# Kernel tuning notes

Measured on AMD Instinct MI355X. Metric: run time of the kernel, lower is better.

## Reference

```python
import jax, jax.numpy as jnp
import numpy as np
from fractions import Fraction
from math import factorial

MUL = 128
LS = [0, 1, 2]  # Rs_in1 = Rs_in2 = [(128,0),(128,1),(128,2)]
D_IN = MUL * sum(2 * l + 1 for l in LS)  # 1152
D_OUT = MUL * sum(2 * lo + 1 for l in LS for lo in range(2 * l + 1))  # 4480
N = 16384


def _su2_cg(j1, m1, j2, m2, j3, m3):
    # SU(2) Clebsch-Gordan coefficient (Racah formula), exact rational arithmetic.
    if m3 != m1 + m2:
        return 0.0
    f = lambda n: factorial(round(n))
    vmin = int(max(-j1 + j2 + m3, -j1 + m1, 0))
    vmax = int(min(j2 + j3 + m1, j3 - j1 + j2, j3 + m3))
    c = ((2.0 * j3 + 1.0) * Fraction(
        f(j3 + j1 - j2) * f(j3 - j1 + j2) * f(j1 + j2 - j3) * f(j3 + m3) * f(j3 - m3),
        f(j1 + j2 + j3 + 1) * f(j1 - m1) * f(j1 + m1) * f(j2 - m2) * f(j2 + m2))) ** 0.5
    s = 0
    for v in range(vmin, vmax + 1):
        s += (-1) ** (v + j2 + m2) * Fraction(
            f(j2 + j3 + m1 - v) * f(j1 - m1 + v),
            f(v) * f(j3 - j1 + j2 - v) * f(j3 + m3 - v) * f(v + j1 - j2 - m3))
    return float(c * s)


def _su2_tensor(j1, j2, j3):
    C = np.zeros((2 * j1 + 1, 2 * j2 + 1, 2 * j3 + 1))
    for m1 in range(-j1, j1 + 1):
        for m2 in range(-j2, j2 + 1):
            m3 = m1 + m2
            if abs(m3) <= j3:
                C[j1 + m1, j2 + m2, j3 + m3] = _su2_cg(j1, m1, j2, m2, j3, m3)
    return C


def _cb(l):
    # change of basis real -> complex spherical harmonics (e3nn convention, incl. (-i)^l phase)
    q = np.zeros((2 * l + 1, 2 * l + 1), dtype=np.complex128)
    for m in range(-l, 0):
        q[l + m, l + abs(m)] = 2 ** -0.5
        q[l + m, l - abs(m)] = -1j * 2 ** -0.5
    q[l, l] = 1.0
    for m in range(1, l + 1):
        q[l + m, l + abs(m)] = (-1) ** m * 2 ** -0.5
        q[l + m, l - abs(m)] = 1j * (-1) ** m * 2 ** -0.5
    return (-1j) ** l * q


def _wigner3j(l1, l2, l3):
    # real-basis Wigner 3j tensor, unit Frobenius norm (e3nn convention)
    C = _su2_tensor(l1, l2, l3).astype(np.complex128)
    C = np.einsum('ij,kl,mn,ikn->jlm', _cb(l1), _cb(l2), np.conj(_cb(l3).T), C)
    C = np.real(C)
    return C / np.linalg.norm(C)


# precomputed CG blocks with 'component' normalization: w3j(l_out, l, l) * sqrt(2*l_out+1)
CG = {(lo, l): jnp.asarray((_wigner3j(lo, l, l) * np.sqrt(2 * lo + 1)).astype(np.float32))
      for l in LS for lo in range(2 * l + 1)}


def _forward(features_1, features_2):
    # elementwise (channel-matched) tensor product, block-sparse CG contraction.
    # Equivalent to: outer(features_1, features_2) then sparse Wigner-3j mixing matmul,
    # but without materializing the [N, d1, d2] outer product.
    lead = features_1.shape[:-1]
    outs = []
    off = 0
    for l in LS:
        d = MUL * (2 * l + 1)
        b1 = features_1[..., off:off + d].reshape(*lead, MUL, 2 * l + 1)
        b2 = features_2[..., off:off + d].reshape(*lead, MUL, 2 * l + 1)
        for lo in range(2 * l + 1):  # selection_rule: l_out in |l-l|..2l, ascending
            o = jnp.einsum('kij,...ui,...uj->...uk', CG[(lo, l)], b1, b2)
            outs.append(o.reshape(*lead, MUL * (2 * lo + 1)))
        off += d
    return jnp.concatenate(outs, axis=-1)  # [..., D_OUT]


def setup_inputs() -> dict:
    key = jax.random.key(0)
    k1, k2 = jax.random.split(key)
    return {
        "features_1": jax.random.normal(k1, (N, D_IN), dtype=jnp.float32),
        "features_2": jax.random.normal(k2, (N, D_IN), dtype=jnp.float32),
    }


def reference(features_1, features_2):
    return _forward(features_1, features_2)
```

## Files before the change

kernel.cpp:

```cpp
#include <hip/hip_runtime.h>


#define NROW 16384
#define DIN  1152
#define DOUT 4480

__device__ float g_cgtab[707];

struct cd { double x, y; };
__device__ __forceinline__ cd cmul(cd a, cd b) {
    return cd{a.x * b.x - a.y * b.y, a.x * b.y + a.y * b.x};
}

__device__ __forceinline__ int imax(int a, int b) { return a > b ? a : b; }
__device__ __forceinline__ int imin(int a, int b) { return a < b ? a : b; }

__device__ double su2_cg_d(int j1, int m1, int j2, int m2, int j3, int m3,
                           const double* f) {
    if (m3 != m1 + m2) return 0.0;
    int vmin = imax(imax(-j1 + j2 + m3, -j1 + m1), 0);
    int vmax = imin(imin(j2 + j3 + m1, j3 - j1 + j2), j3 + m3);
    if (vmax < vmin) return 0.0;
    double c = sqrt((2.0 * j3 + 1.0) *
                    f[j3 + j1 - j2] * f[j3 - j1 + j2] * f[j1 + j2 - j3] *
                    f[j3 + m3] * f[j3 - m3] /
                    (f[j1 + j2 + j3 + 1] * f[j1 - m1] * f[j1 + m1] *
                     f[j2 - m2] * f[j2 + m2]));
    double s = 0.0;
    for (int v = vmin; v <= vmax; ++v) {
        double num = f[j2 + j3 + m1 - v] * f[j1 - m1 + v];
        double den = f[v] * f[j3 - j1 + j2 - v] * f[j3 + m3 - v] * f[v + j1 - j2 - m3];
        double term = num / den;
        s += ((v + j2 + m2) & 1) ? -term : term;
    }
    return c * s;
}

__device__ void fill_cb(int l, cd* q) {
    int d = 2 * l + 1;
    for (int i = 0; i < d * d; i++) q[i] = cd{0.0, 0.0};
    const double is2 = 0.70710678118654752440;
    for (int m = -l; m < 0; m++) {
        q[(l + m) * d + (l - m)] = cd{is2, 0.0};
        q[(l + m) * d + (l + m)] = cd{0.0, -is2};
    }
    q[l * d + l] = cd{1.0, 0.0};
    for (int m = 1; m <= l; m++) {
        double sg = (m & 1) ? -1.0 : 1.0;
        q[(l + m) * d + (l + m)] = cd{sg * is2, 0.0};
        q[(l + m) * d + (l - m)] = cd{0.0, sg * is2};
    }
    int ph = l & 3;
    for (int i = 0; i < d * d; i++) {
        cd z = q[i], r;
        if (ph == 0) r = z;
        else if (ph == 1) r = cd{z.y, -z.x};
        else if (ph == 2) r = cd{-z.x, -z.y};
        else r = cd{-z.y, z.x};
        q[i] = r;
    }
}

__global__ void cg_gen() {
    int b = blockIdx.x;
    int l = (b == 0) ? 0 : (b < 4 ? 1 : 2);
    int lo = (b == 0) ? 0 : (b < 4 ? b - 1 : b - 4);
    int base = (l == 0) ? 0 : (l == 1 ? 1 : 82);
    int d2 = 2 * l + 1, d1 = 2 * lo + 1;
    int off = base + d2 * d2 * lo * lo;
    int Nent = d1 * d2 * d2;

    __shared__ double fct[12];
    __shared__ double su2[225];
    __shared__ cd cb1[81];
    __shared__ cd cb2[25];
    __shared__ double val[225];

    if (threadIdx.x == 0) {
        fct[0] = 1.0;
        for (int i = 1; i < 12; i++) fct[i] = fct[i - 1] * i;
    }
    __syncthreads();

    for (int e = threadIdx.x; e < Nent; e += blockDim.x) {
        int i = e / (d2 * d2), r = e % (d2 * d2);
        int k = r / d2, n = r % d2;
        su2[e] = su2_cg_d(lo, i - lo, l, k - l, l, n - l, fct);
    }
    if (threadIdx.x == 0) { fill_cb(lo, cb1); fill_cb(l, cb2); }
    __syncthreads();

    for (int e = threadIdx.x; e < Nent; e += blockDim.x) {
        int jo = e / (d2 * d2), r = e % (d2 * d2);
        int kb = r / d2, mb = r % d2;
        double sx = 0.0;
        for (int i = 0; i < d1; i++) {
            cd c1 = cb1[i * d1 + jo];
            for (int k = 0; k < d2; k++) {
                cd c12 = cmul(c1, cb2[k * d2 + kb]);
                for (int n = 0; n < d2; n++) {
                    double cv = su2[(i * d2 + k) * d2 + n];
                    if (cv != 0.0) {
                        cd c3 = cb2[n * d2 + mb];
                        c3.y = -c3.y;
                        cd term = cmul(c12, c3);
                        sx += term.x * cv;
                    }
                }
            }
        }
        val[e] = sx;
    }
    __syncthreads();

    double ss = 0.0;
    for (int e = 0; e < Nent; e++) { double v = val[e]; ss += v * v; }
    double scale = sqrt((double)d1) / sqrt(ss);
    for (int e = threadIdx.x; e < Nent; e += blockDim.x)
        g_cgtab[off + e] = (float)(val[e] * scale);
}


template <int DO_, int NE>
__device__ __forceinline__ void contractP(const float* __restrict__ t,
                                          const float* q,
                                          float* __restrict__ os) {
#pragma unroll
    for (int k = 0; k < DO_; k++) {
        float acc = 0.0f;
#pragma unroll
        for (int e = 0; e < NE; e++) acc = fmaf(t[k * NE + e], q[e], acc);
        os[k] = acc;
    }
}

__global__ __launch_bounds__(256, 6) void etp_main(
    const float* __restrict__ f1, const float* __restrict__ f2,
    float* __restrict__ out) {
    __shared__ alignas(16) float os[4096];
    const float* __restrict__ t = g_cgtab;

    const int tid = threadIdx.x;
    const int ch = tid & 127;
    const size_t row = blockIdx.x;

    const float* __restrict__ p1 = f1 + row * DIN;
    const float* __restrict__ p2 = f2 + row * DIN;
    float* __restrict__ po = out + row * DOUT;

    if (tid < 128) {
        float a0 = p1[ch], b0 = p2[ch];
        float a1[3], b1[3];
#pragma unroll
        for (int k = 0; k < 3; k++) {
            a1[k] = p1[128 + ch * 3 + k];
            b1[k] = p2[128 + ch * 3 + k];
        }
        float a2[5], b2[5];
#pragma unroll
        for (int k = 0; k < 5; k++) {
            a2[k] = p1[512 + ch * 5 + k];
            b2[k] = p2[512 + ch * 5 + k];
        }

        po[ch] = t[0] * a0 * b0;

        float q1[9];
#pragma unroll
        for (int i = 0; i < 3; i++)
#pragma unroll
            for (int j = 0; j < 3; j++) q1[i * 3 + j] = a1[i] * b1[j];
        {
            float s = 0.0f;
#pragma unroll
            for (int e = 0; e < 9; e++) s = fmaf(t[1 + e], q1[e], s);
            po[128 + ch] = s;
        }
        contractP<3, 9>(t + 10, q1, os + 0 + ch * 3);
        contractP<5, 9>(t + 37, q1, os + 384 + ch * 5);

        float q2[25];
#pragma unroll
        for (int i = 0; i < 5; i++)
#pragma unroll
            for (int j = 0; j < 5; j++) q2[i * 5 + j] = a2[i] * b2[j];
        contractP<9, 25>(t + 482, q2, os + 2944 + ch * 9);
    } else {
        float a2[5], b2[5];
#pragma unroll
        for (int k = 0; k < 5; k++) {
            a2[k] = p1[512 + ch * 5 + k];
            b2[k] = p2[512 + ch * 5 + k];
        }
        float q2[25];
#pragma unroll
        for (int i = 0; i < 5; i++)
#pragma unroll
            for (int j = 0; j < 5; j++) q2[i * 5 + j] = a2[i] * b2[j];
        {
            float s = 0.0f;
#pragma unroll
            for (int e = 0; e < 25; e++) s = fmaf(t[82 + e], q2[e], s);
            po[1280 + ch] = s;
        }
        contractP<3, 25>(t + 107, q2, os + 1024 + ch * 3);
        contractP<5, 25>(t + 182, q2, os + 1408 + ch * 5);
        contractP<7, 25>(t + 307, q2, os + 2048 + ch * 7);
    }

    __syncthreads();

    const float4* __restrict__ src = reinterpret_cast<const float4*>(os);
    float4* __restrict__ dA = reinterpret_cast<float4*>(po + 256);
    float4* __restrict__ dB = reinterpret_cast<float4*>(po + 1408);
    dA[tid] = src[tid];
#pragma unroll
    for (int i = 1; i < 4; i++) dB[tid + 256 * (i - 1)] = src[tid + 256 * i];
}

extern "C" void kernel_launch(void* const* d_in, const int* in_sizes, int n_in,
                              void* d_out, int out_size, void* d_ws, size_t ws_size,
                              hipStream_t stream) {
    const float* f1 = (const float*)d_in[0];
    const float* f2 = (const float*)d_in[1];
    float* out = (float*)d_out;

    hipLaunchKernelGGL(cg_gen, dim3(9), dim3(256), 0, stream);
    hipLaunchKernelGGL(etp_main, dim3(NROW), dim3(256), 0, stream,
                       f1, f2, out);
}
```

Measured before the change: 428.2 us.

## Compute CG table on host and rebalance per-thread work in main kernel

Replaces the device-side cg_gen kernel with a host computation of the 707-entry CG table, copied asynchronously into the device symbol before the main launch. This removes a small serial GPU kernel from the timed stream, adding a small H2D copy and host work instead. In etp_main, the l=2 input loads and outer product now run in both halves of the block, and the l_out=0 contraction of the l=2 block moves from the upper 128 threads to the lower 128. This evens out the FMA count between the two thread halves.

```diff
diff --git a/kernel.cpp b/kernel.cpp
--- a/kernel.cpp
+++ b/kernel.cpp
@@ -1,4 +1,5 @@
 #include <hip/hip_runtime.h>
+#include <cmath>
 
 
 #define NROW 16384
@@ -7,25 +8,28 @@
 
 __device__ float g_cgtab[707];
 
+namespace cghost {
+
 struct cd { double x, y; };
-__device__ __forceinline__ cd cmul(cd a, cd b) {
+static inline cd cmul(cd a, cd b) {
     return cd{a.x * b.x - a.y * b.y, a.x * b.y + a.y * b.x};
 }
-
-__device__ __forceinline__ int imax(int a, int b) { return a > b ? a : b; }
-__device__ __forceinline__ int imin(int a, int b) { return a < b ? a : b; }
-
-__device__ double su2_cg_d(int j1, int m1, int j2, int m2, int j3, int m3,
-                           const double* f) {
+static inline int imax(int a, int b) { return a > b ? a : b; }
+static inline int imin(int a, int b) { return a < b ? a : b; }
+
+static double fct[12];
+
+static double su2_cg(int j1, int m1, int j2, int m2, int j3, int m3) {
     if (m3 != m1 + m2) return 0.0;
+    const double* f = fct;
     int vmin = imax(imax(-j1 + j2 + m3, -j1 + m1), 0);
     int vmax = imin(imin(j2 + j3 + m1, j3 - j1 + j2), j3 + m3);
     if (vmax < vmin) return 0.0;
-    double c = sqrt((2.0 * j3 + 1.0) *
-                    f[j3 + j1 - j2] * f[j3 - j1 + j2] * f[j1 + j2 - j3] *
-                    f[j3 + m3] * f[j3 - m3] /
-                    (f[j1 + j2 + j3 + 1] * f[j1 - m1] * f[j1 + m1] *
-                     f[j2 - m2] * f[j2 + m2]));
+    double c = std::sqrt((2.0 * j3 + 1.0) *
+                         f[j3 + j1 - j2] * f[j3 - j1 + j2] * f[j1 + j2 - j3] *
+                         f[j3 + m3] * f[j3 - m3] /
+                         (f[j1 + j2 + j3 + 1] * f[j1 - m1] * f[j1 + m1] *
+                          f[j2 - m2] * f[j2 + m2]));
     double s = 0.0;
     for (int v = vmin; v <= vmax; ++v) {
         double num = f[j2 + j3 + m1 - v] * f[j1 - m1 + v];
@@ -36,7 +40,7 @@
     return c * s;
 }
 
-__device__ void fill_cb(int l, cd* q) {
+static void fill_cb(int l, cd* q) {
     int d = 2 * l + 1;
     for (int i = 0; i < d * d; i++) q[i] = cd{0.0, 0.0};
     const double is2 = 0.70710678118654752440;
@@ -61,64 +65,62 @@
     }
 }
 
-__global__ void cg_gen() {
-    int b = blockIdx.x;
-    int l = (b == 0) ? 0 : (b < 4 ? 1 : 2);
-    int lo = (b == 0) ? 0 : (b < 4 ? b - 1 : b - 4);
-    int base = (l == 0) ? 0 : (l == 1 ? 1 : 82);
-    int d2 = 2 * l + 1, d1 = 2 * lo + 1;
-    int off = base + d2 * d2 * lo * lo;
-    int Nent = d1 * d2 * d2;
-
-    __shared__ double fct[12];
-    __shared__ double su2[225];
-    __shared__ cd cb1[81];
-    __shared__ cd cb2[25];
-    __shared__ double val[225];
-
-    if (threadIdx.x == 0) {
-        fct[0] = 1.0;
-        for (int i = 1; i < 12; i++) fct[i] = fct[i - 1] * i;
-    }
-    __syncthreads();
-
-    for (int e = threadIdx.x; e < Nent; e += blockDim.x) {
-        int i = e / (d2 * d2), r = e % (d2 * d2);
-        int k = r / d2, n = r % d2;
-        su2[e] = su2_cg_d(lo, i - lo, l, k - l, l, n - l, fct);
-    }
-    if (threadIdx.x == 0) { fill_cb(lo, cb1); fill_cb(l, cb2); }
-    __syncthreads();
-
-    for (int e = threadIdx.x; e < Nent; e += blockDim.x) {
-        int jo = e / (d2 * d2), r = e % (d2 * d2);
-        int kb = r / d2, mb = r % d2;
-        double sx = 0.0;
-        for (int i = 0; i < d1; i++) {
-            cd c1 = cb1[i * d1 + jo];
-            for (int k = 0; k < d2; k++) {
-                cd c12 = cmul(c1, cb2[k * d2 + kb]);
-                for (int n = 0; n < d2; n++) {
-                    double cv = su2[(i * d2 + k) * d2 + n];
-                    if (cv != 0.0) {
-                        cd c3 = cb2[n * d2 + mb];
-                        c3.y = -c3.y;
-                        cd term = cmul(c12, c3);
-                        sx += term.x * cv;
+static void build(float* tab) {
+    fct[0] = 1.0;
+    for (int i = 1; i < 12; i++) fct[i] = fct[i - 1] * i;
+
+    for (int b = 0; b < 9; b++) {
+        int l = (b == 0) ? 0 : (b < 4 ? 1 : 2);
+        int lo = (b == 0) ? 0 : (b < 4 ? b - 1 : b - 4);
+        int base = (l == 0) ? 0 : (l == 1 ? 1 : 82);
+        int d2 = 2 * l + 1, d1 = 2 * lo + 1;
+        int off = base + d2 * d2 * lo * lo;
+        int Nent = d1 * d2 * d2;
+
+        double su2[225];
+        cd cb1[81], cb2[25];
+        double val[225];
+
+        for (int e = 0; e < Nent; e++) {
+            int i = e / (d2 * d2), r = e % (d2 * d2);
+            int k = r / d2, n = r % d2;
+            su2[e] = su2_cg(lo, i - lo, l, k - l, l, n - l);
+        }
+        fill_cb(lo, cb1);
+        fill_cb(l, cb2);
+
+        for (int e = 0; e < Nent; e++) {
+            int jo = e / (d2 * d2), r = e % (d2 * d2);
+            int kb = r / d2, mb = r % d2;
+            double sx = 0.0;
+            for (int i = 0; i < d1; i++) {
+                cd c1 = cb1[i * d1 + jo];
+                for (int k = 0; k < d2; k++) {
+                    cd c12 = cmul(c1, cb2[k * d2 + kb]);
+                    for (int n = 0; n < d2; n++) {
+                        double cv = su2[(i * d2 + k) * d2 + n];
+                        if (cv != 0.0) {
+                            cd c3 = cb2[n * d2 + mb];
+                            c3.y = -c3.y;
+                            cd term = cmul(c12, c3);
+                            sx += term.x * cv;
+                        }
                     }
                 }
             }
-        }
-        val[e] = sx;
-    }
-    __syncthreads();
-
-    double ss = 0.0;
-    for (int e = 0; e < Nent; e++) { double v = val[e]; ss += v * v; }
-    double scale = sqrt((double)d1) / sqrt(ss);
-    for (int e = threadIdx.x; e < Nent; e += blockDim.x)
-        g_cgtab[off + e] = (float)(val[e] * scale);
-}
+            val[e] = sx;
+        }
+
+        double ss = 0.0;
+        for (int e = 0; e < Nent; e++) ss += val[e] * val[e];
+        double scale = std::sqrt((double)d1) / std::sqrt(ss);
+        for (int e = 0; e < Nent; e++) tab[off + e] = (float)(val[e] * scale);
+    }
+}
+
+}
+
+static float h_cgtab[707];
 
 
 template <int DO_, int NE>
@@ -148,23 +150,28 @@
     const float* __restrict__ p2 = f2 + row * DIN;
     float* __restrict__ po = out + row * DOUT;
 
+    float a2[5], b2[5];
+#pragma unroll
+    for (int k = 0; k < 5; k++) {
+        a2[k] = p1[512 + ch * 5 + k];
+        b2[k] = p2[512 + ch * 5 + k];
+    }
+    float q2[25];
+#pragma unroll
+    for (int i = 0; i < 5; i++)
+#pragma unroll
+        for (int j = 0; j < 5; j++) q2[i * 5 + j] = a2[i] * b2[j];
+
     if (tid < 128) {
         float a0 = p1[ch], b0 = p2[ch];
+        po[ch] = t[0] * a0 * b0;
+
         float a1[3], b1[3];
 #pragma unroll
         for (int k = 0; k < 3; k++) {
             a1[k] = p1[128 + ch * 3 + k];
             b1[k] = p2[128 + ch * 3 + k];
         }
-        float a2[5], b2[5];
-#pragma unroll
-        for (int k = 0; k < 5; k++) {
-            a2[k] = p1[512 + ch * 5 + k];
-            b2[k] = p2[512 + ch * 5 + k];
-        }
-
-        po[ch] = t[0] * a0 * b0;
-
         float q1[9];
 #pragma unroll
         for (int i = 0; i < 3; i++)
@@ -178,31 +185,14 @@
         }
         contractP<3, 9>(t + 10, q1, os + 0 + ch * 3);
         contractP<5, 9>(t + 37, q1, os + 384 + ch * 5);
-
-        float q2[25];
-#pragma unroll
-        for (int i = 0; i < 5; i++)
-#pragma unroll
-            for (int j = 0; j < 5; j++) q2[i * 5 + j] = a2[i] * b2[j];
+        {
+            float s = 0.0f;
+#pragma unroll
+            for (int e = 0; e < 25; e++) s = fmaf(t[82 + e], q2[e], s);
+            po[1280 + ch] = s;
+        }
         contractP<9, 25>(t + 482, q2, os + 2944 + ch * 9);
     } else {
-        float a2[5], b2[5];
-#pragma unroll
-        for (int k = 0; k < 5; k++) {
-            a2[k] = p1[512 + ch * 5 + k];
-            b2[k] = p2[512 + ch * 5 + k];
-        }
-        float q2[25];
-#pragma unroll
-        for (int i = 0; i < 5; i++)
-#pragma unroll
-            for (int j = 0; j < 5; j++) q2[i * 5 + j] = a2[i] * b2[j];
-        {
-            float s = 0.0f;
-#pragma unroll
-            for (int e = 0; e < 25; e++) s = fmaf(t[82 + e], q2[e], s);
-            po[1280 + ch] = s;
-        }
         contractP<3, 25>(t + 107, q2, os + 1024 + ch * 3);
         contractP<5, 25>(t + 182, q2, os + 1408 + ch * 5);
         contractP<7, 25>(t + 307, q2, os + 2048 + ch * 7);
@@ -225,7 +215,12 @@
     const float* f2 = (const float*)d_in[1];
     float* out = (float*)d_out;
 
-    hipLaunchKernelGGL(cg_gen, dim3(9), dim3(256), 0, stream);
+    cghost::build(h_cgtab);
+    void* d_tab = nullptr;
+    hipGetSymbolAddress(&d_tab, HIP_SYMBOL(g_cgtab));
+    hipMemcpyAsync(d_tab, h_cgtab, sizeof(h_cgtab), hipMemcpyHostToDevice,
+                   stream);
+
     hipLaunchKernelGGL(etp_main, dim3(NROW), dim3(256), 0, stream,
                        f1, f2, out);
 }
```

Measured after the change: 396.2 us. -7.5%, faster.
